# Optimization experiments

Measured on AMD Instinct MI355X. Metric: run time of the kernel, lower is better.

The kernel has to match this reference:

```python
import jax, jax.numpy as jnp
import numpy as np

B, Q, K = 8, 128, 1024
QK_DIM = 512   # query_size == key_size
HID = 256      # hidden_size
VDIM = 512     # value feature dim
NEG = -1e6     # mask fill value used by the torch code


def setup_inputs() -> dict:
    key = jax.random.key(0)
    ks = jax.random.split(key, 7)
    queries = jax.random.normal(ks[0], (B, Q, QK_DIM), dtype=jnp.float32)
    keys = jax.random.normal(ks[1], (B, K, QK_DIM), dtype=jnp.float32)
    values = jax.random.normal(ks[2], (B, K, VDIM), dtype=jnp.float32)
    valid_lens = jax.random.randint(ks[3], (B,), 1, K + 1, dtype=jnp.int32)
    # Linear weights (no bias); scaled like torch default init
    Wq = jax.random.normal(ks[4], (QK_DIM, HID), dtype=jnp.float32) / np.sqrt(QK_DIM)
    Wk = jax.random.normal(ks[5], (QK_DIM, HID), dtype=jnp.float32) / np.sqrt(QK_DIM)
    wv = jax.random.normal(ks[6], (HID,), dtype=jnp.float32) / np.sqrt(HID)
    return {"queries": queries, "keys": keys, "values": values,
            "valid_lens": valid_lens, "Wq": Wq, "Wk": Wk, "wv": wv}


def reference(queries, keys, values, valid_lens, Wq, Wk, wv):
    q = jnp.einsum('bqd,dh->bqh', queries, Wq)          # [B,Q,H]
    k = jnp.einsum('bkd,dh->bkh', keys, Wk)             # [B,K,H]
    # broadcast add -> tanh -> score projection
    features = jnp.tanh(q[:, :, None, :] + k[:, None, :, :])  # [B,Q,K,H]
    scores = jnp.einsum('bqkh,h->bqk', features, wv)    # [B,Q,K]
    # masked softmax over last axis (valid_lens per batch row)
    mask = jnp.arange(scores.shape[-1])[None, None, :] < valid_lens[:, None, None]
    scores = jnp.where(mask, scores, NEG)
    attn = jax.nn.softmax(scores, axis=-1)              # [B,Q,K]
    # dropout is identity in eval mode (p=0)
    return jnp.einsum('bqk,bkv->bqv', attn, values)     # [B,Q,VDIM]
```

## Files before the change

kernel.cpp:

```cpp
#include <hip/hip_runtime.h>
#include <math.h>

#define NB 8
#define NQ 128
#define NK 1024
#define ND 512
#define NH 256
#define NV 512

typedef __attribute__((ext_vector_type(8))) short short8v;
typedef __attribute__((ext_vector_type(4))) float floatx4;

__device__ __forceinline__ ushort f2bf(float f) {
  union { float f; unsigned u; } v; v.f = f;
  unsigned r = (v.u + 0x7FFF + ((v.u >> 16) & 1)) >> 16;
  return (ushort)r;
}
__device__ __forceinline__ float bf2f(ushort b) {
  union { unsigned u; float f; } v; v.u = ((unsigned)b) << 16;
  return v.f;
}
__device__ __forceinline__ float wave_rsum(float v) {
#pragma unroll
  for (int off = 32; off; off >>= 1) v += __shfl_xor(v, off);
  return v;
}

__global__ __launch_bounds__(256) void splitw_kernel(
    const float* __restrict__ Wq, const float* __restrict__ Wk,
    ushort* __restrict__ WtQh, ushort* __restrict__ WtQl,
    ushort* __restrict__ WtKh, ushort* __restrict__ WtKl) {
  const int t = threadIdx.x;
  const int mat = blockIdx.x >> 7;
  const int bi = blockIdx.x & 127;
  const int d0 = (bi >> 3) * 32, h0 = (bi & 7) * 32;
  const float* W = mat ? Wk : Wq;
  ushort* Oh = mat ? WtKh : WtQh;
  ushort* Ol = mat ? WtKl : WtQl;
  __shared__ float tile[32][33];
#pragma unroll
  for (int i = 0; i < 4; ++i) {
    int idx = t + 256 * i;
    int r = idx >> 5, c = idx & 31;
    tile[r][c] = W[(size_t)(d0 + r) * NH + h0 + c];
  }
  __syncthreads();
#pragma unroll
  for (int i = 0; i < 4; ++i) {
    int idx = t + 256 * i;
    int hh = idx >> 5, dd = idx & 31;
    float f = tile[dd][hh];
    ushort hi = f2bf(f);
    float lo = f - bf2f(hi);
    Oh[(size_t)(h0 + hh) * ND + d0 + dd] = hi;
    Ol[(size_t)(h0 + hh) * ND + d0 + dd] = f2bf(lo);
  }
}

__global__ __launch_bounds__(256) void convert_v_kernel(
    const float* __restrict__ values, const int* __restrict__ valid_lens,
    ushort* __restrict__ VhT) {
  const int b = blockIdx.z;
  const int k0 = blockIdx.x * 32;
  const int v0 = blockIdx.y * 32;
  const int V = valid_lens[b];
  if (k0 >= ((V + 31) & ~31)) return;
  const int t = threadIdx.x;
  __shared__ float tile[32][33];
#pragma unroll
  for (int i = 0; i < 4; ++i) {
    int idx = t + 256 * i;
    int kk = idx >> 5, vv = idx & 31;
    tile[kk][vv] = values[(size_t)(b * NK + k0 + kk) * NV + v0 + vv];
  }
  __syncthreads();
#pragma unroll
  for (int i = 0; i < 4; ++i) {
    int idx = t + 256 * i;
    int vv = idx >> 5, kk = idx & 31;
    VhT[(size_t)(b * NV + v0 + vv) * NK + k0 + kk] = f2bf(tile[kk][vv]);
  }
}

__global__ __launch_bounds__(64) void proj_mfma_kernel(
    const float* __restrict__ queries, const float* __restrict__ keys,
    const ushort* __restrict__ WtQh, const ushort* __restrict__ WtQl,
    const ushort* __restrict__ WtKh, const ushort* __restrict__ WtKl,
    const int* __restrict__ valid_lens,
    float* __restrict__ Eq, ushort* __restrict__ EkTb) {
  const int lane = threadIdx.x;
  const int lr = lane & 15;
  const int lg = lane >> 4;
  const int bx = blockIdx.x;
  const bool isQ = bx < 64;
  const float* A;
  const ushort *Wh, *Wl;
  int arow0, b = 0, rin = 0;
  if (isQ) {
    A = queries; Wh = WtQh; Wl = WtQl; arow0 = bx * 16;
  } else {
    int kt = bx - 64;
    b = kt >> 6; rin = (kt & 63) * 16;
    if (rin >= valid_lens[b]) return;
    A = keys; Wh = WtKh; Wl = WtKl; arow0 = b * NK + rin;
  }
  const size_t arow = (size_t)(arow0 + lr) * ND;
  const int c0w = blockIdx.y * 64;

  floatx4 acc[4];
#pragma unroll
  for (int cf = 0; cf < 4; ++cf) acc[cf] = (floatx4){0.f, 0.f, 0.f, 0.f};

#pragma unroll 4
  for (int kk = 0; kk < 16; ++kk) {
    const int d0 = kk * 32 + lg * 8;
    float4 a0 = *(const float4*)&A[arow + d0];
    float4 a1 = *(const float4*)&A[arow + d0 + 4];
    float av[8] = {a0.x, a0.y, a0.z, a0.w, a1.x, a1.y, a1.z, a1.w};
    short8v ah, al;
#pragma unroll
    for (int j = 0; j < 8; ++j) {
      ushort h = f2bf(av[j]);
      ah[j] = (short)h;
      al[j] = (short)f2bf(av[j] - bf2f(h));
    }
#pragma unroll
    for (int cf = 0; cf < 4; ++cf) {
      const size_t wrow = (size_t)(c0w + cf * 16 + lr) * ND + d0;
      short8v bh = *(const short8v*)&Wh[wrow];
      short8v bl = *(const short8v*)&Wl[wrow];
      acc[cf] = __builtin_amdgcn_mfma_f32_16x16x32_bf16(al, bh, acc[cf], 0, 0, 0);
      acc[cf] = __builtin_amdgcn_mfma_f32_16x16x32_bf16(ah, bl, acc[cf], 0, 0, 0);
      acc[cf] = __builtin_amdgcn_mfma_f32_16x16x32_bf16(ah, bh, acc[cf], 0, 0, 0);
    }
  }

  const float C2 = 2.885390081777927f;
  if (isQ) {
#pragma unroll
    for (int cf = 0; cf < 4; ++cf) {
      const int h = c0w + cf * 16 + lr;
#pragma unroll
      for (int reg = 0; reg < 4; ++reg) {
        const int row = arow0 + lg * 4 + reg;
        float p = fminf(fmaxf(acc[cf][reg], -15.f), 15.f);
        Eq[(size_t)row * NH + h] = exp2f(p * C2);
      }
    }
  } else {
#pragma unroll
    for (int cf = 0; cf < 4; ++cf) {
      const int h = c0w + cf * 16 + lr;
      ushort4 e;
      e.x = f2bf(exp2f(fminf(fmaxf(acc[cf][0], -15.f), 15.f) * C2));
      e.y = f2bf(exp2f(fminf(fmaxf(acc[cf][1], -15.f), 15.f) * C2));
      e.z = f2bf(exp2f(fminf(fmaxf(acc[cf][2], -15.f), 15.f) * C2));
      e.w = f2bf(exp2f(fminf(fmaxf(acc[cf][3], -15.f), 15.f) * C2));
      *(ushort4*)&EkTb[((size_t)(b * NH + h)) * NK + rin + lg * 4] = e;
    }
  }
}

__global__ __launch_bounds__(256) void score_kernel(
    const float* __restrict__ Eq, const ushort* __restrict__ EkTb,
    const float* __restrict__ wvp, const int* __restrict__ valid_lens,
    ushort* __restrict__ Pb, float* __restrict__ rowsum) {
  const int b = blockIdx.z;
  const int V = valid_lens[b];
  const int k0 = blockIdx.y * 256;
  if (k0 >= V) return;
  const int t = threadIdx.x;
  const int q0 = blockIdx.x * 2;
  const int lane = t & 63, wid = t >> 6;
  const float L2E2 = 2.8853900817779268f;

  __shared__ __align__(16) float eqs[2][NH];
  __shared__ float wvs[NH];
  __shared__ float red[8];

  if (t < 128)
    ((float4*)eqs)[t] = ((const float4*)&Eq[(size_t)(b * NQ + q0) * NH])[t];
  wvs[t] = wvp[t];
  __syncthreads();

  float mn = wave_rsum(fminf(wvs[t], 0.f));
  if (lane == 0) red[wid] = mn;
  __syncthreads();
  const float SN = -(red[0] + red[1] + red[2] + red[3]);
  __syncthreads();

  float acc0 = 0.f, acc1 = 0.f;
  const ushort* ek = EkTb + (size_t)b * NH * NK + k0 + t;
#pragma unroll 8
  for (int h = 0; h < NH; ++h) {
    const float e = bf2f(ek[(size_t)h * NK]);
    const float w = wvs[h];
    acc0 += w * __builtin_amdgcn_rcpf(__builtin_fmaf(eqs[0][h], e, 1.f));
    acc1 += w * __builtin_amdgcn_rcpf(__builtin_fmaf(eqs[1][h], e, 1.f));
  }

  const int k = k0 + t;
  const float p0 = (k < V) ? exp2f(-L2E2 * (acc0 + SN)) : 0.f;
  const float p1 = (k < V) ? exp2f(-L2E2 * (acc1 + SN)) : 0.f;
  const ushort u0 = f2bf(p0), u1 = f2bf(p1);
  Pb[(size_t)(b * NQ + q0) * NK + k] = u0;
  Pb[(size_t)(b * NQ + q0 + 1) * NK + k] = u1;

  float s0 = wave_rsum(bf2f(u0));
  float s1 = wave_rsum(bf2f(u1));
  if (lane == 0) { red[wid] = s0; red[4 + wid] = s1; }
  __syncthreads();
  if (t == 0) {
    atomicAdd(&rowsum[b * NQ + q0], red[0] + red[1] + red[2] + red[3]);
    atomicAdd(&rowsum[b * NQ + q0 + 1], red[4] + red[5] + red[6] + red[7]);
  }
}

__global__ __launch_bounds__(128) void pv_mfma_kernel(
    const ushort* __restrict__ Pb, const ushort* __restrict__ VhT,
    const float* __restrict__ rowsum, const int* __restrict__ valid_lens,
    float* __restrict__ out) {
  const int w = threadIdx.x >> 6;
  const int lane = threadIdx.x & 63;
  const int lr = lane & 15, lg = lane >> 4;
  const int qt = blockIdx.x, vt = blockIdx.y, b = blockIdx.z;
  const int V = valid_lens[b];
  const int Kt = (V + 31) >> 5;
  const int q0 = qt * 16;
  const int v0 = vt * 32 + w * 16;
  const size_t prow = (size_t)(b * NQ + q0 + lr) * NK + lg * 8;
  const size_t vrow = (size_t)(b * NV + v0 + lr) * NK + lg * 8;

  floatx4 accA = (floatx4){0.f, 0.f, 0.f, 0.f};
  floatx4 accB = (floatx4){0.f, 0.f, 0.f, 0.f};
  int s = 0;
  for (; s + 2 <= Kt; s += 2) {
    short8v a0 = *(const short8v*)&Pb[prow + (size_t)s * 32];
    short8v b0 = *(const short8v*)&VhT[vrow + (size_t)s * 32];
    short8v a1 = *(const short8v*)&Pb[prow + (size_t)s * 32 + 32];
    short8v b1 = *(const short8v*)&VhT[vrow + (size_t)s * 32 + 32];
    accA = __builtin_amdgcn_mfma_f32_16x16x32_bf16(a0, b0, accA, 0, 0, 0);
    accB = __builtin_amdgcn_mfma_f32_16x16x32_bf16(a1, b1, accB, 0, 0, 0);
  }
  if (s < Kt) {
    short8v a0 = *(const short8v*)&Pb[prow + (size_t)s * 32];
    short8v b0 = *(const short8v*)&VhT[vrow + (size_t)s * 32];
    accA = __builtin_amdgcn_mfma_f32_16x16x32_bf16(a0, b0, accA, 0, 0, 0);
  }

#pragma unroll
  for (int reg = 0; reg < 4; ++reg) {
    const int row = b * NQ + q0 + lg * 4 + reg;
    const float rs = __builtin_amdgcn_rcpf(rowsum[row]);
    out[(size_t)row * NV + vt * 32 + w * 16 + lr] = (accA[reg] + accB[reg]) * rs;
  }
}

extern "C" void kernel_launch(void* const* d_in, const int* in_sizes, int n_in,
                              void* d_out, int out_size, void* d_ws, size_t ws_size,
                              hipStream_t stream) {
  const float* queries = (const float*)d_in[0];
  const float* keys    = (const float*)d_in[1];
  const float* values  = (const float*)d_in[2];
  const int*   vlens   = (const int*)d_in[3];
  const float* Wq      = (const float*)d_in[4];
  const float* Wk      = (const float*)d_in[5];
  const float* wv      = (const float*)d_in[6];
  float* out = (float*)d_out;

  char* base = (char*)d_ws;
  ushort* WtQh = (ushort*)base;
  ushort* WtQl = WtQh + NH * ND;
  ushort* WtKh = WtQl + NH * ND;
  ushort* WtKl = WtKh + NH * ND;
  float*  Eq   = (float*)(base + (1 << 20));
  ushort* EkTb = (ushort*)(base + (2 << 20));
  ushort* Pb   = (ushort*)(base + (6 << 20));
  ushort* VhT  = (ushort*)(base + (8 << 20));
  float*  rowsum = (float*)(base + (16 << 20));

  hipMemsetAsync(rowsum, 0, NB * NQ * sizeof(float), stream);
  splitw_kernel<<<dim3(256), dim3(256), 0, stream>>>(Wq, Wk, WtQh, WtQl, WtKh, WtKl);
  convert_v_kernel<<<dim3(32, 16, 8), dim3(256), 0, stream>>>(values, vlens, VhT);
  proj_mfma_kernel<<<dim3(576, 4), dim3(64), 0, stream>>>(
      queries, keys, WtQh, WtQl, WtKh, WtKl, vlens, Eq, EkTb);
  score_kernel<<<dim3(64, 4, 8), dim3(256), 0, stream>>>(
      Eq, EkTb, wv, vlens, Pb, rowsum);
  pv_mfma_kernel<<<dim3(8, 16, 8), dim3(128), 0, stream>>>(
      Pb, VhT, rowsum, vlens, out);
}
```

Before: 179.3 us.

## Share A-tile split in LDS and software-pipeline loads in proj, score, pv kernels

The projection kernel now uses 256-thread blocks, with four waves each covering 64 output columns. The 16-row A tile is split once into bf16 hi/lo parts and staged in LDS, where before each of four blocks re-read and re-split it from global memory. Weight loads are double-buffered across k steps. The score kernel prefetches Ek values in chunks of eight and reads eq/wv as float4 from LDS, and the PV kernel prefetches the next P/V fragments ahead of the MFMAs. The cost is more register pressure and an added LDS barrier.

Result: no change. 181.4 us (+1.2%).

```diff
diff --git a/kernel.cpp b/kernel.cpp
--- a/kernel.cpp
+++ b/kernel.cpp
@@ -82,15 +82,15 @@
   }
 }
 
-__global__ __launch_bounds__(64) void proj_mfma_kernel(
+__global__ __launch_bounds__(256) void proj_mfma_kernel(
     const float* __restrict__ queries, const float* __restrict__ keys,
     const ushort* __restrict__ WtQh, const ushort* __restrict__ WtQl,
     const ushort* __restrict__ WtKh, const ushort* __restrict__ WtKl,
     const int* __restrict__ valid_lens,
     float* __restrict__ Eq, ushort* __restrict__ EkTb) {
-  const int lane = threadIdx.x;
-  const int lr = lane & 15;
-  const int lg = lane >> 4;
+  const int t = threadIdx.x;
+  const int lane = t & 63, wvid = t >> 6;
+  const int lr = lane & 15, lg = lane >> 4;
   const int bx = blockIdx.x;
   const bool isQ = bx < 64;
   const float* A;
@@ -104,36 +104,84 @@
     if (rin >= valid_lens[b]) return;
     A = keys; Wh = WtKh; Wl = WtKl; arow0 = b * NK + rin;
   }
-  const size_t arow = (size_t)(arow0 + lr) * ND;
-  const int c0w = blockIdx.y * 64;
+
+  __shared__ ushort Ah[16][520];
+  __shared__ ushort Al[16][520];
+  {
+    const float* Arow = A + (size_t)arow0 * ND;
+#pragma unroll
+    for (int i = 0; i < 8; ++i) {
+      int e = (t + 256 * i) * 4;
+      int r = e >> 9, c = e & 511;
+      float4 a = *(const float4*)&Arow[e];
+      ushort4 h, l;
+      h.x = f2bf(a.x); l.x = f2bf(a.x - bf2f(h.x));
+      h.y = f2bf(a.y); l.y = f2bf(a.y - bf2f(h.y));
+      h.z = f2bf(a.z); l.z = f2bf(a.z - bf2f(h.z));
+      h.w = f2bf(a.w); l.w = f2bf(a.w - bf2f(h.w));
+      *(ushort4*)&Ah[r][c] = h;
+      *(ushort4*)&Al[r][c] = l;
+    }
+  }
+  __syncthreads();
+
+  const int c0w = wvid * 64;
+  const ushort* Whb = Wh + (size_t)(c0w + lr) * ND + lg * 8;
+  const ushort* Wlb = Wl + (size_t)(c0w + lr) * ND + lg * 8;
 
   floatx4 acc[4];
 #pragma unroll
   for (int cf = 0; cf < 4; ++cf) acc[cf] = (floatx4){0.f, 0.f, 0.f, 0.f};
 
-#pragma unroll 4
-  for (int kk = 0; kk < 16; ++kk) {
-    const int d0 = kk * 32 + lg * 8;
-    float4 a0 = *(const float4*)&A[arow + d0];
-    float4 a1 = *(const float4*)&A[arow + d0 + 4];
-    float av[8] = {a0.x, a0.y, a0.z, a0.w, a1.x, a1.y, a1.z, a1.w};
-    short8v ah, al;
-#pragma unroll
-    for (int j = 0; j < 8; ++j) {
-      ushort h = f2bf(av[j]);
-      ah[j] = (short)h;
-      al[j] = (short)f2bf(av[j] - bf2f(h));
-    }
-#pragma unroll
-    for (int cf = 0; cf < 4; ++cf) {
-      const size_t wrow = (size_t)(c0w + cf * 16 + lr) * ND + d0;
-      short8v bh = *(const short8v*)&Wh[wrow];
-      short8v bl = *(const short8v*)&Wl[wrow];
-      acc[cf] = __builtin_amdgcn_mfma_f32_16x16x32_bf16(al, bh, acc[cf], 0, 0, 0);
-      acc[cf] = __builtin_amdgcn_mfma_f32_16x16x32_bf16(ah, bl, acc[cf], 0, 0, 0);
-      acc[cf] = __builtin_amdgcn_mfma_f32_16x16x32_bf16(ah, bh, acc[cf], 0, 0, 0);
-    }
-  }
+#define LOADW(dsth, dstl, kkv)                                            \
+  {                                                                       \
+    const size_t _d = (size_t)(kkv) * 32;                                 \
+    dsth##0 = *(const short8v*)&Whb[_d];                                  \
+    dstl##0 = *(const short8v*)&Wlb[_d];                                  \
+    dsth##1 = *(const short8v*)&Whb[(size_t)16 * ND + _d];                \
+    dstl##1 = *(const short8v*)&Wlb[(size_t)16 * ND + _d];                \
+    dsth##2 = *(const short8v*)&Whb[(size_t)32 * ND + _d];                \
+    dstl##2 = *(const short8v*)&Wlb[(size_t)32 * ND + _d];                \
+    dsth##3 = *(const short8v*)&Whb[(size_t)48 * ND + _d];                \
+    dstl##3 = *(const short8v*)&Wlb[(size_t)48 * ND + _d];                \
+  }
+
+#define MFMA4(ah_, al_, wh, wl)                                           \
+  {                                                                       \
+    acc[0] = __builtin_amdgcn_mfma_f32_16x16x32_bf16(al_, wh##0, acc[0], 0, 0, 0); \
+    acc[0] = __builtin_amdgcn_mfma_f32_16x16x32_bf16(ah_, wl##0, acc[0], 0, 0, 0); \
+    acc[0] = __builtin_amdgcn_mfma_f32_16x16x32_bf16(ah_, wh##0, acc[0], 0, 0, 0); \
+    acc[1] = __builtin_amdgcn_mfma_f32_16x16x32_bf16(al_, wh##1, acc[1], 0, 0, 0); \
+    acc[1] = __builtin_amdgcn_mfma_f32_16x16x32_bf16(ah_, wl##1, acc[1], 0, 0, 0); \
+    acc[1] = __builtin_amdgcn_mfma_f32_16x16x32_bf16(ah_, wh##1, acc[1], 0, 0, 0); \
+    acc[2] = __builtin_amdgcn_mfma_f32_16x16x32_bf16(al_, wh##2, acc[2], 0, 0, 0); \
+    acc[2] = __builtin_amdgcn_mfma_f32_16x16x32_bf16(ah_, wl##2, acc[2], 0, 0, 0); \
+    acc[2] = __builtin_amdgcn_mfma_f32_16x16x32_bf16(ah_, wh##2, acc[2], 0, 0, 0); \
+    acc[3] = __builtin_amdgcn_mfma_f32_16x16x32_bf16(al_, wh##3, acc[3], 0, 0, 0); \
+    acc[3] = __builtin_amdgcn_mfma_f32_16x16x32_bf16(ah_, wl##3, acc[3], 0, 0, 0); \
+    acc[3] = __builtin_amdgcn_mfma_f32_16x16x32_bf16(ah_, wh##3, acc[3], 0, 0, 0); \
+  }
+
+  short8v wAh0, wAh1, wAh2, wAh3, wAl0, wAl1, wAl2, wAl3;
+  short8v wBh0, wBh1, wBh2, wBh3, wBl0, wBl1, wBl2, wBl3;
+  LOADW(wAh, wAl, 0);
+#pragma unroll 1
+  for (int kk = 0; kk < 16; kk += 2) {
+    LOADW(wBh, wBl, kk + 1);
+    {
+      short8v ah_ = *(const short8v*)&Ah[lr][kk * 32 + lg * 8];
+      short8v al_ = *(const short8v*)&Al[lr][kk * 32 + lg * 8];
+      MFMA4(ah_, al_, wAh, wAl);
+    }
+    if (kk + 2 < 16) LOADW(wAh, wAl, kk + 2);
+    {
+      short8v ah_ = *(const short8v*)&Ah[lr][(kk + 1) * 32 + lg * 8];
+      short8v al_ = *(const short8v*)&Al[lr][(kk + 1) * 32 + lg * 8];
+      MFMA4(ah_, al_, wBh, wBl);
+    }
+  }
+#undef LOADW
+#undef MFMA4
 
   const float C2 = 2.885390081777927f;
   if (isQ) {
@@ -175,7 +223,7 @@
   const float L2E2 = 2.8853900817779268f;
 
   __shared__ __align__(16) float eqs[2][NH];
-  __shared__ float wvs[NH];
+  __shared__ __align__(16) float wvs[NH];
   __shared__ float red[8];
 
   if (t < 128)
@@ -189,15 +237,41 @@
   const float SN = -(red[0] + red[1] + red[2] + red[3]);
   __syncthreads();
 
+  const ushort* ek = EkTb + (size_t)b * NH * NK + k0 + t;
   float acc0 = 0.f, acc1 = 0.f;
-  const ushort* ek = EkTb + (size_t)b * NH * NK + k0 + t;
-#pragma unroll 8
-  for (int h = 0; h < NH; ++h) {
-    const float e = bf2f(ek[(size_t)h * NK]);
-    const float w = wvs[h];
-    acc0 += w * __builtin_amdgcn_rcpf(__builtin_fmaf(eqs[0][h], e, 1.f));
-    acc1 += w * __builtin_amdgcn_rcpf(__builtin_fmaf(eqs[1][h], e, 1.f));
-  }
+
+  ushort uA[8], uB[8];
+#define LOADE(u, h0)                                                      \
+  {                                                                       \
+    _Pragma("unroll") for (int j = 0; j < 8; ++j)                         \
+        u[j] = ek[(size_t)((h0) + j) * NK];                               \
+  }
+#define CHUNK(u, h0)                                                      \
+  {                                                                       \
+    float e0[8], e1[8], w8[8];                                            \
+    *(float4*)&e0[0] = *(const float4*)&eqs[0][(h0)];                     \
+    *(float4*)&e0[4] = *(const float4*)&eqs[0][(h0) + 4];                 \
+    *(float4*)&e1[0] = *(const float4*)&eqs[1][(h0)];                     \
+    *(float4*)&e1[4] = *(const float4*)&eqs[1][(h0) + 4];                 \
+    *(float4*)&w8[0] = *(const float4*)&wvs[(h0)];                        \
+    *(float4*)&w8[4] = *(const float4*)&wvs[(h0) + 4];                    \
+    _Pragma("unroll") for (int j = 0; j < 8; ++j) {                       \
+      const float ev = bf2f(u[j]);                                        \
+      acc0 += w8[j] * __builtin_amdgcn_rcpf(__builtin_fmaf(e0[j], ev, 1.f)); \
+      acc1 += w8[j] * __builtin_amdgcn_rcpf(__builtin_fmaf(e1[j], ev, 1.f)); \
+    }                                                                     \
+  }
+
+  LOADE(uA, 0);
+#pragma unroll 1
+  for (int h0 = 0; h0 < NH; h0 += 16) {
+    LOADE(uB, h0 + 8);
+    CHUNK(uA, h0);
+    if (h0 + 16 < NH) LOADE(uA, h0 + 16);
+    CHUNK(uB, h0 + 8);
+  }
+#undef LOADE
+#undef CHUNK
 
   const int k = k0 + t;
   const float p0 = (k < V) ? exp2f(-L2E2 * (acc0 + SN)) : 0.f;
@@ -228,31 +302,41 @@
   const int Kt = (V + 31) >> 5;
   const int q0 = qt * 16;
   const int v0 = vt * 32 + w * 16;
-  const size_t prow = (size_t)(b * NQ + q0 + lr) * NK + lg * 8;
-  const size_t vrow = (size_t)(b * NV + v0 + lr) * NK + lg * 8;
+  const ushort* pp = Pb + (size_t)(b * NQ + q0 + lr) * NK + lg * 8;
+  const ushort* vp = VhT + (size_t)(b * NV + v0 + lr) * NK + lg * 8;
 
   floatx4 accA = (floatx4){0.f, 0.f, 0.f, 0.f};
   floatx4 accB = (floatx4){0.f, 0.f, 0.f, 0.f};
+  short8v pa, va, pb, vb;
+
+  pa = *(const short8v*)&pp[0];
+  va = *(const short8v*)&vp[0];
+  if (Kt > 1) {
+    pb = *(const short8v*)&pp[32];
+    vb = *(const short8v*)&vp[32];
+  }
   int s = 0;
-  for (; s + 2 <= Kt; s += 2) {
-    short8v a0 = *(const short8v*)&Pb[prow + (size_t)s * 32];
-    short8v b0 = *(const short8v*)&VhT[vrow + (size_t)s * 32];
-    short8v a1 = *(const short8v*)&Pb[prow + (size_t)s * 32 + 32];
-    short8v b1 = *(const short8v*)&VhT[vrow + (size_t)s * 32 + 32];
-    accA = __builtin_amdgcn_mfma_f32_16x16x32_bf16(a0, b0, accA, 0, 0, 0);
-    accB = __builtin_amdgcn_mfma_f32_16x16x32_bf16(a1, b1, accB, 0, 0, 0);
-  }
-  if (s < Kt) {
-    short8v a0 = *(const short8v*)&Pb[prow + (size_t)s * 32];
-    short8v b0 = *(const short8v*)&VhT[vrow + (size_t)s * 32];
-    accA = __builtin_amdgcn_mfma_f32_16x16x32_bf16(a0, b0, accA, 0, 0, 0);
-  }
+  while (s + 2 <= Kt) {
+    accA = __builtin_amdgcn_mfma_f32_16x16x32_bf16(pa, va, accA, 0, 0, 0);
+    if (s + 2 < Kt) {
+      pa = *(const short8v*)&pp[(size_t)(s + 2) * 32];
+      va = *(const short8v*)&vp[(size_t)(s + 2) * 32];
+    }
+    accB = __builtin_amdgcn_mfma_f32_16x16x32_bf16(pb, vb, accB, 0, 0, 0);
+    if (s + 3 < Kt) {
+      pb = *(const short8v*)&pp[(size_t)(s + 3) * 32];
+      vb = *(const short8v*)&vp[(size_t)(s + 3) * 32];
+    }
+    s += 2;
+  }
+  if (s < Kt)
+    accA = __builtin_amdgcn_mfma_f32_16x16x32_bf16(pa, va, accA, 0, 0, 0);
 
 #pragma unroll
   for (int reg = 0; reg < 4; ++reg) {
     const int row = b * NQ + q0 + lg * 4 + reg;
     const float rs = __builtin_amdgcn_rcpf(rowsum[row]);
-    out[(size_t)row * NV + vt * 32 + w * 16 + lr] = (accA[reg] + accB[reg]) * rs;
+    out[(size_t)row * NV + v0 + lr] = (accA[reg] + accB[reg]) * rs;
   }
 }
 
@@ -282,7 +366,7 @@
   hipMemsetAsync(rowsum, 0, NB * NQ * sizeof(float), stream);
   splitw_kernel<<<dim3(256), dim3(256), 0, stream>>>(Wq, Wk, WtQh, WtQl, WtKh, WtKl);
   convert_v_kernel<<<dim3(32, 16, 8), dim3(256), 0, stream>>>(values, vlens, VhT);
-  proj_mfma_kernel<<<dim3(576, 4), dim3(64), 0, stream>>>(
+  proj_mfma_kernel<<<dim3(576), dim3(256), 0, stream>>>(
       queries, keys, WtQh, WtQl, WtKh, WtKl, vlens, Eq, EkTb);
   score_kernel<<<dim3(64, 4, 8), dim3(256), 0, stream>>>(
       Eq, EkTb, wv, vlens, Pb, rowsum);
```
